# Performance work log

Measured on AMD Instinct MI355X. Metric: run time of the kernel, lower is better.

The kernel has to match this reference:

```python
import jax, jax.numpy as jnp
import numpy as np

EPS = 1e-8  # torch.nn.CosineSimilarity default eps


def setup_inputs() -> dict:
    key = jax.random.key(0)
    batch = jax.random.normal(key, (8192, 128), dtype=jnp.float32)
    return {"batch": batch}


def reference(batch):
    B = batch.shape[0]
    # Full pairwise cosine similarity matrix S[i, j]
    norms = jnp.linalg.norm(batch, axis=1)                      # [B]
    denom = jnp.maximum(norms[:, None] * norms[None, :], EPS)   # [B, B]
    S = (batch @ batch.T) / denom                                # [B, B]
    # Denominator of soft_nll(i, j): sum_{m != i} exp(S[i, m])
    expS = jnp.exp(S)
    Z = expS.sum(axis=1) - jnp.diagonal(expS)                    # [B]
    logZ = jnp.log(Z)                                            # [B]
    # term(i, j) = -log( exp(S[i,j]) / Z_i ) = -S[i,j] + logZ_i
    # Original loop: for k in 1..(B+1)//2 - 1, pairs (2k-1, 2k) 1-indexed
    N = (B + 1) // 2
    ks = jnp.arange(1, N)
    i = 2 * ks - 2  # 0-indexed first element of pair
    j = 2 * ks - 1  # 0-indexed second element of pair
    pair_loss = (-S[i, j] + logZ[i]) + (-S[j, i] + logZ[j])
    return jnp.sum(pair_loss) / B
```

## Files before the change

### kernel.cpp

```cpp
#include <hip/hip_runtime.h>
#include <hip/hip_bf16.h>

typedef __attribute__((ext_vector_type(8))) short short8;
typedef __attribute__((ext_vector_type(4))) float floatx4;

#define B_ROWS 8192
#define DIM 128
#define NPAIR 4095
#define RSCALE 1.2011224087864498f

#define GLOAD_LDS16(gp, lp)                                                     \
    __builtin_amdgcn_global_load_lds(                                           \
        (const __attribute__((address_space(1))) void*)(gp),                    \
        (__attribute__((address_space(3))) void*)(lp), 16, 0, 0)

__global__ void kzero(float* __restrict__ Z) {
    int i = blockIdx.x * 256 + threadIdx.x;
    if (i < B_ROWS) Z[i] = 0.f;
}

__global__ void kprep(const float* __restrict__ X, __hip_bfloat16* __restrict__ XN,
                      float* __restrict__ pairT, float* __restrict__ out) {
    __shared__ float2 lds[4][64];
    const int wid = threadIdx.x >> 6;
    const int lane = threadIdx.x & 63;
    const int row = blockIdx.x * 4 + wid;

    const float2 v = *reinterpret_cast<const float2*>(X + row * DIM + lane * 2);
    float ss = v.x * v.x + v.y * v.y;
    #pragma unroll
    for (int m = 1; m < 64; m <<= 1) ss += __shfl_xor(ss, m, 64);
    const float rn = ss > 0.f ? rsqrtf(ss) : 0.f;
    const float2 nv = make_float2(v.x * rn, v.y * rn);

    *reinterpret_cast<__hip_bfloat162*>(XN + row * DIM + lane * 2) =
        __float22bfloat162_rn(make_float2(nv.x * RSCALE, nv.y * RSCALE));
    lds[wid][lane] = nv;
    __syncthreads();

    if ((wid & 1) == 0) {
        const int p = blockIdx.x * 2 + (wid >> 1);
        if (p < NPAIR) {
            const float2 a = lds[wid][lane];
            const float2 b = lds[wid + 1][lane];
            float d = a.x * b.x + a.y * b.y;
            #pragma unroll
            for (int m = 1; m < 64; m <<= 1) d += __shfl_xor(d, m, 64);
            if (lane == 0) pairT[p] = d;
        }
    }
    if (blockIdx.x == 0 && threadIdx.x == 0) out[0] = 0.f;
}

__device__ __forceinline__ void stage_half(const __hip_bfloat16* __restrict__ gsrc,
                                           __hip_bfloat16* lbuf, int tid) {
    const int wid = tid >> 6;
    const int lane = tid & 63;
    #pragma unroll
    for (int it = 0; it < 4; ++it) {
        const int woff = it * 2048 + wid * 512;
        const int e = woff + lane * 8;
        const int src = (e & ~127) | ((e & 127) ^ (((e >> 7) & 7) << 3));
        GLOAD_LDS16(gsrc + src, lbuf + woff);
    }
}

template <bool USEP>
__global__ void __launch_bounds__(256, 2) kgemm(const __hip_bfloat16* __restrict__ XN,
                                                float* __restrict__ ZP) {
    __shared__ __hip_bfloat16 Bs[2][64 * DIM];

    const int tid = threadIdx.x;
    const int wid = tid >> 6;
    const int lane = tid & 63;
    const int lr = lane & 15;
    const int lk = lane >> 4;
    const int wr = wid >> 1;
    const int wc = wid & 1;
    const int rb = blockIdx.y;
    const int g = blockIdx.x;

    short8 a[4][4];
    const __hip_bfloat16* Abase = XN + (rb * 128 + wr * 64 + lr) * DIM + lk * 8;
    #pragma unroll
    for (int m = 0; m < 4; ++m)
        #pragma unroll
        for (int kk = 0; kk < 4; ++kk)
            a[kk][m] = *reinterpret_cast<const short8*>(Abase + m * 16 * DIM + kk * 32);

    float rp[4][4];
    #pragma unroll
    for (int m = 0; m < 4; ++m)
        #pragma unroll
        for (int r = 0; r < 4; ++r) rp[m][r] = 0.f;

    const floatx4 zero4 = {0.f, 0.f, 0.f, 0.f};

    stage_half(XN + (g * 4) * 128 * DIM, Bs[0], tid);
    __syncthreads();

    #pragma unroll 2
    for (int t = 0; t < 8; ++t) {
        const int cur = t & 1;
        if (t < 7) {
            const int nt = t + 1;
            stage_half(XN + ((g * 4 + (nt >> 1)) * 128 + (nt & 1) * 64) * DIM,
                       Bs[cur ^ 1], tid);
        }

        const int cbj = g * 4 + (t >> 1);
        const bool dzero = (cbj == rb) && ((t & 1) == wr);
        const __hip_bfloat16* Bt = Bs[cur];

        short8 b[4][2];
        #pragma unroll
        for (int n = 0; n < 2; ++n) {
            const int row = wc * 32 + n * 16 + lr;
            #pragma unroll
            for (int kk = 0; kk < 4; ++kk) {
                const int col = (kk * 32 + lk * 8) ^ ((row & 7) << 3);
                b[kk][n] = *reinterpret_cast<const short8*>(&Bt[row * DIM + col]);
            }
        }

        floatx4 acc[4][2];
        #pragma unroll
        for (int m = 0; m < 4; ++m)
            #pragma unroll
            for (int n = 0; n < 2; ++n)
                acc[m][n] = __builtin_amdgcn_mfma_f32_16x16x32_bf16(a[0][m], b[0][n], zero4, 0, 0, 0);
        #pragma unroll
        for (int kk = 1; kk < 4; ++kk)
            #pragma unroll
            for (int m = 0; m < 4; ++m)
                #pragma unroll
                for (int n = 0; n < 2; ++n)
                    acc[m][n] = __builtin_amdgcn_mfma_f32_16x16x32_bf16(a[kk][m], b[kk][n], acc[m][n], 0, 0, 0);

        if (dzero) {
            #pragma unroll
            for (int m = 0; m < 4; ++m)
                #pragma unroll
                for (int n = 0; n < 2; ++n)
                    #pragma unroll
                    for (int r = 0; r < 4; ++r) {
                        float e = __builtin_amdgcn_exp2f(acc[m][n][r]);
                        if (m * 16 + lk * 4 + r == wc * 32 + n * 16 + lr) e = 0.f;
                        rp[m][r] += e;
                    }
        } else {
            #pragma unroll
            for (int m = 0; m < 4; ++m)
                #pragma unroll
                for (int n = 0; n < 2; ++n)
                    #pragma unroll
                    for (int r = 0; r < 4; ++r)
                        rp[m][r] += __builtin_amdgcn_exp2f(acc[m][n][r]);
        }
        __syncthreads();
    }

    #pragma unroll
    for (int m = 0; m < 4; ++m)
        #pragma unroll
        for (int r = 0; r < 4; ++r) {
            float v = rp[m][r];
            v += __shfl_xor(v, 1, 64);
            v += __shfl_xor(v, 2, 64);
            v += __shfl_xor(v, 4, 64);
            v += __shfl_xor(v, 8, 64);
            if (lr == 0) {
                const int row = rb * 128 + wr * 64 + m * 16 + lk * 4 + r;
                if (USEP)
                    ZP[(g * 2 + wc) * B_ROWS + row] = v;
                else
                    atomicAdd(&ZP[row], v);
            }
        }
}

__global__ void kfinalP(const float* __restrict__ P, const float* __restrict__ pairT,
                        float* __restrict__ out) {
    const int r = blockIdx.x * 256 + threadIdx.x;
    float s = 0.f;
    if (r < B_ROWS - 2) {
        float z = 0.f;
        #pragma unroll
        for (int tt = 0; tt < 32; ++tt) z += P[tt * B_ROWS + r];
        s = logf(z);
    }
    if (r < NPAIR) s -= 2.f * pairT[r];
    #pragma unroll
    for (int m = 1; m < 64; m <<= 1) s += __shfl_xor(s, m, 64);
    __shared__ float red[4];
    const int wid = threadIdx.x >> 6;
    const int lane = threadIdx.x & 63;
    if (lane == 0) red[wid] = s;
    __syncthreads();
    if (threadIdx.x == 0) {
        float tsum = red[0] + red[1] + red[2] + red[3];
        atomicAdd(out, tsum / (float)B_ROWS);
    }
}

__global__ void kfinalZ(const float* __restrict__ Z, const float* __restrict__ pairT,
                        float* __restrict__ out) {
    float s = 0.f;
    for (int r = threadIdx.x; r < B_ROWS - 2; r += 1024) s += logf(Z[r]);
    for (int p = threadIdx.x; p < NPAIR; p += 1024) s -= 2.f * pairT[p];
    #pragma unroll
    for (int m = 1; m < 64; m <<= 1) s += __shfl_xor(s, m, 64);
    __shared__ float red[16];
    const int wid = threadIdx.x >> 6;
    const int lane = threadIdx.x & 63;
    if (lane == 0) red[wid] = s;
    __syncthreads();
    if (threadIdx.x == 0) {
        float t = 0.f;
        #pragma unroll
        for (int i = 0; i < 16; ++i) t += red[i];
        out[0] = t / (float)B_ROWS;
    }
}

extern "C" void kernel_launch(void* const* d_in, const int* in_sizes, int n_in,
                              void* d_out, int out_size, void* d_ws, size_t ws_size,
                              hipStream_t stream) {
    (void)in_sizes; (void)n_in; (void)out_size;
    const float* X = (const float*)d_in[0];
    float* out = (float*)d_out;
    char* ws = (char*)d_ws;

    float* Z = (float*)ws;
    float* pairT = (float*)(ws + 32768);
    __hip_bfloat16* XN = (__hip_bfloat16*)(ws + 49152);
    float* P = (float*)(ws + 49152 + 2097152);
    const size_t need = 49152 + 2097152 + (size_t)32 * B_ROWS * 4;
    const bool useP = ws_size >= need;

    kprep<<<2048, 256, 0, stream>>>(X, XN, pairT, out);
    if (useP) {
        kgemm<true><<<dim3(16, 64), 256, 0, stream>>>(XN, P);
        kfinalP<<<32, 256, 0, stream>>>(P, pairT, out);
    } else {
        kzero<<<32, 256, 0, stream>>>(Z);
        kgemm<false><<<dim3(16, 64), 256, 0, stream>>>(XN, Z);
        kfinalZ<<<1, 1024, 0, stream>>>(Z, pairT, out);
    }
}
```

Measured before the change: 39.22 us.

## Shrink GEMM blocks to two waves sharing 32-column B tiles, add setprio

Restructures the fused similarity/exp-sum kernel so each block has two waves, each owning 64 rows, and both stream the same 32-column B tiles through a smaller double-buffered LDS buffer. The grid doubles to 32x64 blocks, each covering 256 columns, which keeps the partial-sum slot count at 32. It also raises wave priority around the MFMA section. The aim is more blocks and smaller LDS use for better occupancy and latency hiding. The cost is that each staged B tile is reused by only two waves instead of four, and the column loop is no longer unrolled.

Measured after the change: 44.67 us. +13.9%, slower.

```diff
diff --git a/kernel.cpp b/kernel.cpp
--- a/kernel.cpp
+++ b/kernel.cpp
@@ -7,6 +7,7 @@
 #define B_ROWS 8192
 #define DIM 128
 #define NPAIR 4095
+#define NSLOT 32
 #define RSCALE 1.2011224087864498f
 
 #define GLOAD_LDS16(gp, lp)                                                     \
@@ -52,13 +53,13 @@
     if (blockIdx.x == 0 && threadIdx.x == 0) out[0] = 0.f;
 }
 
-__device__ __forceinline__ void stage_half(const __hip_bfloat16* __restrict__ gsrc,
-                                           __hip_bfloat16* lbuf, int tid) {
+__device__ __forceinline__ void stage32(const __hip_bfloat16* __restrict__ gsrc,
+                                        __hip_bfloat16* lbuf, int tid) {
     const int wid = tid >> 6;
     const int lane = tid & 63;
     #pragma unroll
     for (int it = 0; it < 4; ++it) {
-        const int woff = it * 2048 + wid * 512;
+        const int woff = it * 1024 + wid * 512;
         const int e = woff + lane * 8;
         const int src = (e & ~127) | ((e & 127) ^ (((e >> 7) & 7) << 3));
         GLOAD_LDS16(gsrc + src, lbuf + woff);
@@ -66,22 +67,20 @@
 }
 
 template <bool USEP>
-__global__ void __launch_bounds__(256, 2) kgemm(const __hip_bfloat16* __restrict__ XN,
-                                                float* __restrict__ ZP) {
-    __shared__ __hip_bfloat16 Bs[2][64 * DIM];
+__global__ void __launch_bounds__(128) kgemm(const __hip_bfloat16* __restrict__ XN,
+                                             float* __restrict__ ZP) {
+    __shared__ __hip_bfloat16 Bs[2][32 * DIM];
 
     const int tid = threadIdx.x;
-    const int wid = tid >> 6;
+    const int w = tid >> 6;
     const int lane = tid & 63;
     const int lr = lane & 15;
     const int lk = lane >> 4;
-    const int wr = wid >> 1;
-    const int wc = wid & 1;
     const int rb = blockIdx.y;
     const int g = blockIdx.x;
 
     short8 a[4][4];
-    const __hip_bfloat16* Abase = XN + (rb * 128 + wr * 64 + lr) * DIM + lk * 8;
+    const __hip_bfloat16* Abase = XN + (rb * 128 + w * 64 + lr) * DIM + lk * 8;
     #pragma unroll
     for (int m = 0; m < 4; ++m)
         #pragma unroll
@@ -95,27 +94,26 @@
         for (int r = 0; r < 4; ++r) rp[m][r] = 0.f;
 
     const floatx4 zero4 = {0.f, 0.f, 0.f, 0.f};
-
-    stage_half(XN + (g * 4) * 128 * DIM, Bs[0], tid);
-    __syncthreads();
-
-    #pragma unroll 2
-    for (int t = 0; t < 8; ++t) {
-        const int cur = t & 1;
-        if (t < 7) {
-            const int nt = t + 1;
-            stage_half(XN + ((g * 4 + (nt >> 1)) * 128 + (nt & 1) * 64) * DIM,
-                       Bs[cur ^ 1], tid);
-        }
-
-        const int cbj = g * 4 + (t >> 1);
-        const bool dzero = (cbj == rb) && ((t & 1) == wr);
+    const int R0 = rb * 2 + w;
+
+    stage32(XN + (size_t)(g * 256) * DIM, Bs[0], tid);
+    __syncthreads();
+
+    for (int s = 0; s < 8; ++s) {
+        const int cur = s & 1;
+        if (s < 7)
+            stage32(XN + (size_t)(g * 256 + (s + 1) * 32) * DIM, Bs[cur ^ 1], tid);
+
         const __hip_bfloat16* Bt = Bs[cur];
-
+        const int C0 = g * 256 + s * 32;
+        const bool dzero = ((C0 >> 6) == R0);
+        const int coff = C0 & 32;
+
+        __builtin_amdgcn_s_setprio(1);
         short8 b[4][2];
         #pragma unroll
         for (int n = 0; n < 2; ++n) {
-            const int row = wc * 32 + n * 16 + lr;
+            const int row = n * 16 + lr;
             #pragma unroll
             for (int kk = 0; kk < 4; ++kk) {
                 const int col = (kk * 32 + lk * 8) ^ ((row & 7) << 3);
@@ -136,6 +134,7 @@
                 #pragma unroll
                 for (int n = 0; n < 2; ++n)
                     acc[m][n] = __builtin_amdgcn_mfma_f32_16x16x32_bf16(a[kk][m], b[kk][n], acc[m][n], 0, 0, 0);
+        __builtin_amdgcn_s_setprio(0);
 
         if (dzero) {
             #pragma unroll
@@ -145,7 +144,7 @@
                     #pragma unroll
                     for (int r = 0; r < 4; ++r) {
                         float e = __builtin_amdgcn_exp2f(acc[m][n][r]);
-                        if (m * 16 + lk * 4 + r == wc * 32 + n * 16 + lr) e = 0.f;
+                        if (m * 16 + lk * 4 + r == coff + n * 16 + lr) e = 0.f;
                         rp[m][r] += e;
                     }
         } else {
@@ -170,9 +169,9 @@
             v += __shfl_xor(v, 4, 64);
             v += __shfl_xor(v, 8, 64);
             if (lr == 0) {
-                const int row = rb * 128 + wr * 64 + m * 16 + lk * 4 + r;
+                const int row = rb * 128 + w * 64 + m * 16 + lk * 4 + r;
                 if (USEP)
-                    ZP[(g * 2 + wc) * B_ROWS + row] = v;
+                    ZP[g * B_ROWS + row] = v;
                 else
                     atomicAdd(&ZP[row], v);
             }
@@ -186,7 +185,7 @@
     if (r < B_ROWS - 2) {
         float z = 0.f;
         #pragma unroll
-        for (int tt = 0; tt < 32; ++tt) z += P[tt * B_ROWS + r];
+        for (int tt = 0; tt < NSLOT; ++tt) z += P[tt * B_ROWS + r];
         s = logf(z);
     }
     if (r < NPAIR) s -= 2.f * pairT[r];
@@ -235,16 +234,16 @@
     float* pairT = (float*)(ws + 32768);
     __hip_bfloat16* XN = (__hip_bfloat16*)(ws + 49152);
     float* P = (float*)(ws + 49152 + 2097152);
-    const size_t need = 49152 + 2097152 + (size_t)32 * B_ROWS * 4;
+    const size_t need = 49152 + 2097152 + (size_t)NSLOT * B_ROWS * 4;
     const bool useP = ws_size >= need;
 
     kprep<<<2048, 256, 0, stream>>>(X, XN, pairT, out);
     if (useP) {
-        kgemm<true><<<dim3(16, 64), 256, 0, stream>>>(XN, P);
+        kgemm<true><<<dim3(32, 64), 128, 0, stream>>>(XN, P);
         kfinalP<<<32, 256, 0, stream>>>(P, pairT, out);
     } else {
         kzero<<<32, 256, 0, stream>>>(Z);
-        kgemm<false><<<dim3(16, 64), 256, 0, stream>>>(XN, Z);
+        kgemm<false><<<dim3(32, 64), 128, 0, stream>>>(XN, Z);
         kfinalZ<<<1, 1024, 0, stream>>>(Z, pairT, out);
     }
 }
```
